# Kernel optimization log

Hardware: AMD Instinct MI355X
Metric: run time of the kernel (lower is better)

Reference implementation:

```python
import jax, jax.numpy as jnp
import numpy as np

EPS = 1e-12  # torch F.normalize eps


def setup_inputs() -> dict:
    key = jax.random.key(0)
    ks = jax.random.split(key, 6)
    B, N, P, H = 32, 512, 8, 300
    node_attr = jax.random.normal(ks[0], (B, N, P, H), dtype=jnp.float32)
    edge_attr = jax.random.normal(ks[1], (B, 1, 1, H), dtype=jnp.float32)  # unused for ins_id=0
    instruction = jax.random.normal(ks[2], (B, H), dtype=jnp.float32)
    distribution = jax.random.uniform(ks[3], (B, N), dtype=jnp.float32)  # unused for ins_id=0
    node_prop_similarities = jax.random.uniform(ks[4], (B, P), dtype=jnp.float32)
    node_mask = jnp.zeros((B, N), dtype=jnp.float32)
    # weight_node_properties initialized as stacked identities; perturb to be nontrivial
    W_node = jnp.tile(jnp.eye(H, dtype=jnp.float32)[None], (P, 1, 1)) \
        + 0.02 * jax.random.normal(ks[5], (P, H, H), dtype=jnp.float32)
    w_state = jnp.ones((H,), dtype=jnp.float32)  # weight_state_score init = ones
    return {
        "node_attr": node_attr,
        "edge_attr": edge_attr,
        "instruction": instruction,
        "distribution": distribution,
        "ins_id": 0,
        "node_prop_similarities": node_prop_similarities,
        "node_mask": node_mask,
        "W_node": W_node,
        "w_state": w_state,
    }


def reference(node_attr, edge_attr, instruction, distribution, ins_id,
              node_prop_similarities, node_mask, W_node, w_state):
    # n_ins=3, ins_id=0 branch of NSMCell.forward
    # node_attr: (B,N,P,H) -> (B,P,N,H)
    x = jnp.transpose(node_attr, (0, 2, 1, 3))
    # broadcast-multiply instruction, then per-property matmul with W_node[p]
    y = instruction[:, None, None, :] * x                      # (B,P,N,H)
    z = jnp.einsum('bpnh,phk->bpnk', y, W_node)                # (B,P,N,H)
    z = z * node_prop_similarities[:, :, None, None]           # weight by property similarity
    # torch F.normalize default dim=1 -> L2-normalize over the P axis
    norm = jnp.sqrt(jnp.sum(z * z, axis=1, keepdims=True))
    z = z / jnp.maximum(norm, EPS)
    s = jnp.sum(z, axis=1)                                     # (B,N,H) sum over P
    node_scores = jax.nn.elu(s)                                # dropout p=0 -> identity
    scores = jnp.einsum('bnh,h->bn', node_scores, w_state)     # (B,N)
    return jax.nn.softmax(scores + node_mask, axis=1)
```

## Files before the change

kernel.cpp:

```cpp
#include <hip/hip_runtime.h>

#define B 32
#define N 512
#define P 8
#define H 300
#define EPSN 1e-12f
#define NT 32
#define NB (N / NT)
#define SAP 344

typedef _Float16 f16x8 __attribute__((ext_vector_type(8)));
typedef float f32x4 __attribute__((ext_vector_type(4)));

__global__ __launch_bounds__(256)
void nsm_prep(const float* __restrict__ node_attr,
              const float* __restrict__ instruction,
              const float* __restrict__ W,
              _Float16* __restrict__ afrag,
              _Float16* __restrict__ wfrag)
{
    const int t = threadIdx.x;
    const int z = blockIdx.z;

    if (z == P) {
        const int idx = blockIdx.y * NB + blockIdx.x;
        const int fb  = idx * 4 + (t >> 6);
        if (fb >= 1600) return;
        const int lane = t & 63;
        const int p  = fb / 200;
        const int rm = fb % 200;
        const int ht = rm / 20;
        const int kt = rm % 20;
        const int k  = kt * 16 + (lane & 15);
        const int h0 = ht * 32 + (lane >> 4) * 8;
        f16x8 v;
        #pragma unroll
        for (int j = 0; j < 8; ++j) {
            int h = h0 + j;
            float wv = (h < H && k < H) ? W[((size_t)p * H + h) * H + k] : 0.f;
            v[j] = (_Float16)wv;
        }
        *(f16x8*)(wfrag + (size_t)fb * 512 + (size_t)lane * 8) = v;
        return;
    }

    __shared__ _Float16 sA[NT * SAP];
    const int nb = blockIdx.x, b = blockIdx.y, p = z;
    const int r  = t >> 3;
    const int oc = t & 7;

    const float* srcA = node_attr + ((size_t)((b * N + nb * NT + r) * P + p)) * H;
    const float* ins  = instruction + (size_t)b * H;

    #pragma unroll
    for (int i = 0; i < 5; ++i) {
        int o  = oc + i * 8;
        int h0 = o * 8;
        f16x8 v8;
        #pragma unroll
        for (int j = 0; j < 8; ++j) v8[j] = (_Float16)0.f;
        if (o < 37) {
            float4 va = *(const float4*)(srcA + h0);
            float4 vb = *(const float4*)(srcA + h0 + 4);
            float4 sa = *(const float4*)(ins + h0);
            float4 sb = *(const float4*)(ins + h0 + 4);
            v8[0] = (_Float16)(va.x * sa.x); v8[1] = (_Float16)(va.y * sa.y);
            v8[2] = (_Float16)(va.z * sa.z); v8[3] = (_Float16)(va.w * sa.w);
            v8[4] = (_Float16)(vb.x * sb.x); v8[5] = (_Float16)(vb.y * sb.y);
            v8[6] = (_Float16)(vb.z * sb.z); v8[7] = (_Float16)(vb.w * sb.w);
        } else if (o == 37) {
            float4 va = *(const float4*)(srcA + h0);
            float4 sa = *(const float4*)(ins + h0);
            v8[0] = (_Float16)(va.x * sa.x); v8[1] = (_Float16)(va.y * sa.y);
            v8[2] = (_Float16)(va.z * sa.z); v8[3] = (_Float16)(va.w * sa.w);
        }
        *(f16x8*)&sA[r * SAP + h0] = v8;
    }
    __syncthreads();

    const int w = t >> 6, l = t & 63;
    const size_t ub = ((size_t)(b * NB + nb) * P + p) * 20;
    #pragma unroll
    for (int uu = 0; uu < 5; ++uu) {
        int u  = w + uu * 4;
        int ht = u >> 1, nt = u & 1;
        f16x8 v = *(const f16x8*)&sA[(nt * 16 + (l & 15)) * SAP + ht * 32 + (l >> 4) * 8];
        *(f16x8*)(afrag + (ub + u) * 512 + (size_t)l * 8) = v;
    }
}

__global__ __launch_bounds__(256, 2)
void nsm_scores_mfma(const _Float16* __restrict__ afrag,
                     const _Float16* __restrict__ wfrag,
                     const float* __restrict__ nps,
                     const float* __restrict__ w_state,
                     float* __restrict__ pscore)
{
    const int t  = threadIdx.x;
    const int nb = blockIdx.x;
    const int b  = blockIdx.y;
    const int w  = t >> 6;
    const int l  = t & 63;

    const _Float16* Ab = afrag + ((size_t)(b * NB + nb) * P) * 10240 + (size_t)l * 8;
    const _Float16* Wb = wfrag + (size_t)(w * 5) * 512 + (size_t)l * 8;

    f32x4 S1[2][5], S2[2][5];
    #pragma unroll
    for (int nt = 0; nt < 2; ++nt)
        #pragma unroll
        for (int kt = 0; kt < 5; ++kt) {
            S1[nt][kt] = (f32x4){0.f, 0.f, 0.f, 0.f};
            S2[nt][kt] = (f32x4){0.f, 0.f, 0.f, 0.f};
        }

    f16x8 abuf[2][2], wbuf[2][5];
    #pragma unroll
    for (int s = 0; s < 2; ++s) {
        abuf[s][0] = *(const f16x8*)(Ab + s * 1024);
        abuf[s][1] = *(const f16x8*)(Ab + s * 1024 + 512);
        #pragma unroll
        for (int kt = 0; kt < 5; ++kt)
            wbuf[s][kt] = *(const f16x8*)(Wb + (size_t)s * 10240 + kt * 512);
    }

    for (int p = 0; p < P; ++p) {
        f32x4 acc[2][5];
        #pragma unroll
        for (int nt = 0; nt < 2; ++nt)
            #pragma unroll
            for (int kt = 0; kt < 5; ++kt)
                acc[nt][kt] = (f32x4){0.f, 0.f, 0.f, 0.f};

        #pragma unroll
        for (int ht = 0; ht < 10; ++ht) {
            const int sl = ht & 1;
            #pragma unroll
            for (int kt = 0; kt < 5; ++kt) {
                acc[0][kt] = __builtin_amdgcn_mfma_f32_16x16x32_f16(abuf[sl][0], wbuf[sl][kt], acc[0][kt], 0, 0, 0);
                acc[1][kt] = __builtin_amdgcn_mfma_f32_16x16x32_f16(abuf[sl][1], wbuf[sl][kt], acc[1][kt], 0, 0, 0);
            }
            if (ht < 8 || p < 7) {
                const int s2 = p * 10 + ht + 2;
                const _Float16* Ap2 = Ab + (size_t)s2 * 1024;
                const _Float16* Wp2 = Wb + (size_t)s2 * 10240;
                abuf[sl][0] = *(const f16x8*)(Ap2);
                abuf[sl][1] = *(const f16x8*)(Ap2 + 512);
                #pragma unroll
                for (int kt = 0; kt < 5; ++kt)
                    wbuf[sl][kt] = *(const f16x8*)(Wp2 + kt * 512);
            }
        }

        const float sim = nps[b * P + p];
        #pragma unroll
        for (int nt = 0; nt < 2; ++nt)
            #pragma unroll
            for (int kt = 0; kt < 5; ++kt) {
                f32x4 z = acc[nt][kt] * sim;
                S1[nt][kt] += z;
                S2[nt][kt] += z * z;
            }
    }

    #pragma unroll
    for (int nt = 0; nt < 2; ++nt) {
        #pragma unroll
        for (int j = 0; j < 4; ++j) {
            float part = 0.f;
            #pragma unroll
            for (int kt = 0; kt < 5; ++kt) {
                int k = w * 80 + kt * 16 + (l & 15);
                if (k < H) {
                    float s1 = S1[nt][kt][j];
                    float s2 = S2[nt][kt][j];
                    float denom = fmaxf(sqrtf(s2), EPSN);
                    float v = s1 / denom;
                    float e = v > 0.f ? v : expm1f(v);
                    part += e * w_state[k];
                }
            }
            part += __shfl_xor(part, 1, 16);
            part += __shfl_xor(part, 2, 16);
            part += __shfl_xor(part, 4, 16);
            part += __shfl_xor(part, 8, 16);
            if ((l & 15) == 0) {
                int row = nt * 16 + (l >> 4) * 4 + j;
                pscore[(size_t)w * (B * N) + (size_t)b * N + nb * NT + row] = part;
            }
        }
    }
}

__global__ __launch_bounds__(256)
void nsm_softmax_kernel(const float* __restrict__ pscore,
                        const float* __restrict__ mask,
                        float* __restrict__ out)
{
    __shared__ float redm[4];
    __shared__ float reds[4];
    const int b = blockIdx.x;
    const int t = threadIdx.x;

    float v0 = mask[b * N + t];
    float v1 = mask[b * N + 256 + t];
    #pragma unroll
    for (int w = 0; w < 4; ++w) {
        v0 += pscore[(size_t)w * (B * N) + b * N + t];
        v1 += pscore[(size_t)w * (B * N) + b * N + 256 + t];
    }

    float m = fmaxf(v0, v1);
    m = fmaxf(m, __shfl_xor(m, 1, 64));
    m = fmaxf(m, __shfl_xor(m, 2, 64));
    m = fmaxf(m, __shfl_xor(m, 4, 64));
    m = fmaxf(m, __shfl_xor(m, 8, 64));
    m = fmaxf(m, __shfl_xor(m, 16, 64));
    m = fmaxf(m, __shfl_xor(m, 32, 64));
    const int wave = t >> 6;
    const int lane = t & 63;
    if (lane == 0) redm[wave] = m;
    __syncthreads();
    m = fmaxf(fmaxf(redm[0], redm[1]), fmaxf(redm[2], redm[3]));

    float e0 = expf(v0 - m);
    float e1 = expf(v1 - m);
    float s = e0 + e1;
    s += __shfl_xor(s, 1, 64);
    s += __shfl_xor(s, 2, 64);
    s += __shfl_xor(s, 4, 64);
    s += __shfl_xor(s, 8, 64);
    s += __shfl_xor(s, 16, 64);
    s += __shfl_xor(s, 32, 64);
    if (lane == 0) reds[wave] = s;
    __syncthreads();
    s = reds[0] + reds[1] + reds[2] + reds[3];

    out[b * N + t]       = e0 / s;
    out[b * N + 256 + t] = e1 / s;
}

extern "C" void kernel_launch(void* const* d_in, const int* in_sizes, int n_in,
                              void* d_out, int out_size, void* d_ws, size_t ws_size,
                              hipStream_t stream)
{
    const float* node_attr   = (const float*)d_in[0];
    const float* instruction = (const float*)d_in[2];
    const float* nps         = (const float*)d_in[5];
    const float* node_mask   = (const float*)d_in[6];
    const float* W_node      = (const float*)d_in[7];
    const float* w_state     = (const float*)d_in[8];
    float* out = (float*)d_out;

    _Float16* afrag = (_Float16*)d_ws;
    _Float16* wfrag = afrag + (size_t)B * NB * P * 20 * 512;
    float*    pscore = (float*)(wfrag + 1600 * 512);

    nsm_prep<<<dim3(NB, B, P + 1), 256, 0, stream>>>(node_attr, instruction,
                                                     W_node, afrag, wfrag);
    nsm_scores_mfma<<<dim3(NB, B), 256, 0, stream>>>(afrag, wfrag, nps, w_state, pscore);
    nsm_softmax_kernel<<<dim3(B), 256, 0, stream>>>(pscore, node_mask, out);
}
```

Baseline: 340.1 us.

## Fuse activation fp16 conversion into MFMA kernel with double-buffered LDS staging

Measured after the change: 357.0 us. 1.05x slower.

```diff
diff --git a/kernel.cpp b/kernel.cpp
--- a/kernel.cpp
+++ b/kernel.cpp
@@ -7,103 +7,97 @@
 #define EPSN 1e-12f
 #define NT 32
 #define NB (N / NT)
-#define SAP 344
 
 typedef _Float16 f16x8 __attribute__((ext_vector_type(8)));
 typedef float f32x4 __attribute__((ext_vector_type(4)));
 
 __global__ __launch_bounds__(256)
-void nsm_prep(const float* __restrict__ node_attr,
-              const float* __restrict__ instruction,
-              const float* __restrict__ W,
-              _Float16* __restrict__ afrag,
-              _Float16* __restrict__ wfrag)
-{
-    const int t = threadIdx.x;
-    const int z = blockIdx.z;
-
-    if (z == P) {
-        const int idx = blockIdx.y * NB + blockIdx.x;
-        const int fb  = idx * 4 + (t >> 6);
-        if (fb >= 1600) return;
-        const int lane = t & 63;
-        const int p  = fb / 200;
-        const int rm = fb % 200;
-        const int ht = rm / 20;
-        const int kt = rm % 20;
-        const int k  = kt * 16 + (lane & 15);
-        const int h0 = ht * 32 + (lane >> 4) * 8;
-        f16x8 v;
-        #pragma unroll
-        for (int j = 0; j < 8; ++j) {
-            int h = h0 + j;
-            float wv = (h < H && k < H) ? W[((size_t)p * H + h) * H + k] : 0.f;
-            v[j] = (_Float16)wv;
-        }
-        *(f16x8*)(wfrag + (size_t)fb * 512 + (size_t)lane * 8) = v;
-        return;
-    }
-
-    __shared__ _Float16 sA[NT * SAP];
-    const int nb = blockIdx.x, b = blockIdx.y, p = z;
-    const int r  = t >> 3;
-    const int oc = t & 7;
-
-    const float* srcA = node_attr + ((size_t)((b * N + nb * NT + r) * P + p)) * H;
-    const float* ins  = instruction + (size_t)b * H;
-
-    #pragma unroll
-    for (int i = 0; i < 5; ++i) {
-        int o  = oc + i * 8;
-        int h0 = o * 8;
-        f16x8 v8;
-        #pragma unroll
-        for (int j = 0; j < 8; ++j) v8[j] = (_Float16)0.f;
-        if (o < 37) {
-            float4 va = *(const float4*)(srcA + h0);
-            float4 vb = *(const float4*)(srcA + h0 + 4);
-            float4 sa = *(const float4*)(ins + h0);
-            float4 sb = *(const float4*)(ins + h0 + 4);
-            v8[0] = (_Float16)(va.x * sa.x); v8[1] = (_Float16)(va.y * sa.y);
-            v8[2] = (_Float16)(va.z * sa.z); v8[3] = (_Float16)(va.w * sa.w);
-            v8[4] = (_Float16)(vb.x * sb.x); v8[5] = (_Float16)(vb.y * sb.y);
-            v8[6] = (_Float16)(vb.z * sb.z); v8[7] = (_Float16)(vb.w * sb.w);
-        } else if (o == 37) {
-            float4 va = *(const float4*)(srcA + h0);
-            float4 sa = *(const float4*)(ins + h0);
-            v8[0] = (_Float16)(va.x * sa.x); v8[1] = (_Float16)(va.y * sa.y);
-            v8[2] = (_Float16)(va.z * sa.z); v8[3] = (_Float16)(va.w * sa.w);
-        }
-        *(f16x8*)&sA[r * SAP + h0] = v8;
-    }
-    __syncthreads();
-
-    const int w = t >> 6, l = t & 63;
-    const size_t ub = ((size_t)(b * NB + nb) * P + p) * 20;
-    #pragma unroll
-    for (int uu = 0; uu < 5; ++uu) {
-        int u  = w + uu * 4;
-        int ht = u >> 1, nt = u & 1;
-        f16x8 v = *(const f16x8*)&sA[(nt * 16 + (l & 15)) * SAP + ht * 32 + (l >> 4) * 8];
-        *(f16x8*)(afrag + (ub + u) * 512 + (size_t)l * 8) = v;
-    }
+void nsm_prep_w(const float* __restrict__ W, _Float16* __restrict__ wfrag)
+{
+    const int gid  = blockIdx.x * 256 + threadIdx.x;
+    const int fb   = gid >> 6;
+    const int lane = gid & 63;
+    const int p  = fb / 200;
+    const int rm = fb % 200;
+    const int ht = rm / 20;
+    const int kt = rm % 20;
+    const int k  = kt * 16 + (lane & 15);
+    const int h0 = ht * 32 + (lane >> 4) * 8;
+
+    f16x8 v;
+    #pragma unroll
+    for (int j = 0; j < 8; ++j) {
+        int h = h0 + j;
+        float wv = (h < H && k < H) ? W[((size_t)p * H + h) * H + k] : 0.f;
+        v[j] = (_Float16)wv;
+    }
+    *(f16x8*)(wfrag + (size_t)fb * 512 + (size_t)lane * 8) = v;
 }
 
 __global__ __launch_bounds__(256, 2)
-void nsm_scores_mfma(const _Float16* __restrict__ afrag,
-                     const _Float16* __restrict__ wfrag,
-                     const float* __restrict__ nps,
-                     const float* __restrict__ w_state,
-                     float* __restrict__ pscore)
-{
+void nsm_fused(const float* __restrict__ node_attr,
+               const float* __restrict__ instruction,
+               const float* __restrict__ nps,
+               const _Float16* __restrict__ wfrag,
+               const float* __restrict__ w_state,
+               float* __restrict__ pscore)
+{
+    __shared__ _Float16 sA[2][20 * 512];
+    __shared__ float sI[320];
+
     const int t  = threadIdx.x;
     const int nb = blockIdx.x;
     const int b  = blockIdx.y;
-    const int w  = t >> 6;
-    const int l  = t & 63;
-
-    const _Float16* Ab = afrag + ((size_t)(b * NB + nb) * P) * 10240 + (size_t)l * 8;
+    const int w  = t >> 6, l = t & 63;
+    const int r  = t >> 3, oc = t & 7;
+
+    for (int i = t; i < 320; i += 256)
+        sI[i] = (i < H) ? instruction[b * H + i] : 0.f;
+
+    const float* srcA = node_attr + ((size_t)(b * N + nb * NT + r) * P) * H;
+    const int szl = (l * 8) ^ (((l >> 4) & 3) << 3);
     const _Float16* Wb = wfrag + (size_t)(w * 5) * 512 + (size_t)l * 8;
+
+    float4 va[5], vb[5];
+
+    auto loadA = [&](int pp) {
+        const float* src = srcA + (size_t)pp * H;
+        #pragma unroll
+        for (int i = 0; i < 5; ++i) {
+            int o = oc + i * 8, h0 = o * 8;
+            va[i] = make_float4(0.f, 0.f, 0.f, 0.f);
+            vb[i] = make_float4(0.f, 0.f, 0.f, 0.f);
+            if (o < 37) {
+                va[i] = *(const float4*)(src + h0);
+                vb[i] = *(const float4*)(src + h0 + 4);
+            } else if (o == 37) {
+                va[i] = *(const float4*)(src + h0);
+            }
+        }
+    };
+    auto convWrite = [&](int buf) {
+        _Float16* dst = sA[buf];
+        #pragma unroll
+        for (int i = 0; i < 5; ++i) {
+            int o = oc + i * 8, h0 = o * 8;
+            float4 sa = *(const float4*)&sI[h0];
+            float4 sb = *(const float4*)&sI[h0 + 4];
+            f16x8 v8;
+            v8[0] = (_Float16)(va[i].x * sa.x); v8[1] = (_Float16)(va[i].y * sa.y);
+            v8[2] = (_Float16)(va[i].z * sa.z); v8[3] = (_Float16)(va[i].w * sa.w);
+            v8[4] = (_Float16)(vb[i].x * sb.x); v8[5] = (_Float16)(vb[i].y * sb.y);
+            v8[6] = (_Float16)(vb[i].z * sb.z); v8[7] = (_Float16)(vb[i].w * sb.w);
+            int u  = (o >> 2) * 2 + (r >> 4);
+            int lw = ((o & 3) << 4) | (r & 15);
+            int off = u * 512 + ((lw * 8) ^ ((o & 3) << 3));
+            *(f16x8*)&dst[off] = v8;
+        }
+    };
+
+    loadA(0);
+    __syncthreads();
+    convWrite(0);
+    __syncthreads();
 
     f32x4 S1[2][5], S2[2][5];
     #pragma unroll
@@ -114,17 +108,12 @@
             S2[nt][kt] = (f32x4){0.f, 0.f, 0.f, 0.f};
         }
 
-    f16x8 abuf[2][2], wbuf[2][5];
-    #pragma unroll
-    for (int s = 0; s < 2; ++s) {
-        abuf[s][0] = *(const f16x8*)(Ab + s * 1024);
-        abuf[s][1] = *(const f16x8*)(Ab + s * 1024 + 512);
-        #pragma unroll
-        for (int kt = 0; kt < 5; ++kt)
-            wbuf[s][kt] = *(const f16x8*)(Wb + (size_t)s * 10240 + kt * 512);
-    }
-
     for (int p = 0; p < P; ++p) {
+        if (p < 7) loadA(p + 1);
+
+        const _Float16* sbuf = sA[p & 1];
+        const _Float16* Wp = Wb + (size_t)(p * 200) * 512;
+
         f32x4 acc[2][5];
         #pragma unroll
         for (int nt = 0; nt < 2; ++nt)
@@ -132,25 +121,31 @@
             for (int kt = 0; kt < 5; ++kt)
                 acc[nt][kt] = (f32x4){0.f, 0.f, 0.f, 0.f};
 
+        f16x8 ab[2][2], wf[2][5];
+        ab[0][0] = *(const f16x8*)&sbuf[0 * 512 + szl];
+        ab[0][1] = *(const f16x8*)&sbuf[1 * 512 + szl];
+        #pragma unroll
+        for (int kt = 0; kt < 5; ++kt)
+            wf[0][kt] = *(const f16x8*)(Wp + (size_t)kt * 512);
+
         #pragma unroll
         for (int ht = 0; ht < 10; ++ht) {
-            const int sl = ht & 1;
-            #pragma unroll
-            for (int kt = 0; kt < 5; ++kt) {
-                acc[0][kt] = __builtin_amdgcn_mfma_f32_16x16x32_f16(abuf[sl][0], wbuf[sl][kt], acc[0][kt], 0, 0, 0);
-                acc[1][kt] = __builtin_amdgcn_mfma_f32_16x16x32_f16(abuf[sl][1], wbuf[sl][kt], acc[1][kt], 0, 0, 0);
-            }
-            if (ht < 8 || p < 7) {
-                const int s2 = p * 10 + ht + 2;
-                const _Float16* Ap2 = Ab + (size_t)s2 * 1024;
-                const _Float16* Wp2 = Wb + (size_t)s2 * 10240;
-                abuf[sl][0] = *(const f16x8*)(Ap2);
-                abuf[sl][1] = *(const f16x8*)(Ap2 + 512);
+            const int cur = ht & 1, nxt = cur ^ 1;
+            if (ht < 9) {
+                ab[nxt][0] = *(const f16x8*)&sbuf[((ht + 1) * 2 + 0) * 512 + szl];
+                ab[nxt][1] = *(const f16x8*)&sbuf[((ht + 1) * 2 + 1) * 512 + szl];
                 #pragma unroll
                 for (int kt = 0; kt < 5; ++kt)
-                    wbuf[sl][kt] = *(const f16x8*)(Wp2 + kt * 512);
-            }
-        }
+                    wf[nxt][kt] = *(const f16x8*)(Wp + (size_t)((ht + 1) * 20 + kt) * 512);
+            }
+            #pragma unroll
+            for (int kt = 0; kt < 5; ++kt) {
+                acc[0][kt] = __builtin_amdgcn_mfma_f32_16x16x32_f16(ab[cur][0], wf[cur][kt], acc[0][kt], 0, 0, 0);
+                acc[1][kt] = __builtin_amdgcn_mfma_f32_16x16x32_f16(ab[cur][1], wf[cur][kt], acc[1][kt], 0, 0, 0);
+            }
+        }
+
+        if (p < 7) convWrite((p + 1) & 1);
 
         const float sim = nps[b * P + p];
         #pragma unroll
@@ -161,6 +156,7 @@
                 S1[nt][kt] += z;
                 S2[nt][kt] += z * z;
             }
+        __syncthreads();
     }
 
     #pragma unroll
@@ -252,12 +248,11 @@
     const float* w_state     = (const float*)d_in[8];
     float* out = (float*)d_out;
 
-    _Float16* afrag = (_Float16*)d_ws;
-    _Float16* wfrag = afrag + (size_t)B * NB * P * 20 * 512;
+    _Float16* wfrag  = (_Float16*)d_ws;
     float*    pscore = (float*)(wfrag + 1600 * 512);
 
-    nsm_prep<<<dim3(NB, B, P + 1), 256, 0, stream>>>(node_attr, instruction,
-                                                     W_node, afrag, wfrag);
-    nsm_scores_mfma<<<dim3(NB, B), 256, 0, stream>>>(afrag, wfrag, nps, w_state, pscore);
+    nsm_prep_w<<<dim3(400), 256, 0, stream>>>(W_node, wfrag);
+    nsm_fused<<<dim3(NB, B), 256, 0, stream>>>(node_attr, instruction, nps,
+                                               wfrag, w_state, pscore);
     nsm_softmax_kernel<<<dim3(B), 256, 0, stream>>>(pscore, node_mask, out);
 }
```
